# Kernel optimization log

Hardware: AMD Instinct MI355X
Metric: run time of the kernel (lower is better)

The kernel has to match this reference:

```python
import jax, jax.numpy as jnp
import numpy as np

B, H, S, DH = 2, 16, 2048, 64
MASK_FILL = -10000.0


def setup_inputs() -> dict:
    key = jax.random.key(0)
    kq, kk, kv = jax.random.split(key, 3)
    q = jax.random.normal(kq, (B, H, S, DH), dtype=jnp.float32)
    k = jax.random.normal(kk, (B, H, S, DH), dtype=jnp.float32)
    v = jax.random.normal(kv, (B, H, S, DH), dtype=jnp.float32)
    # causal mask: True where attention is disallowed (upper triangle)
    mask = jnp.triu(jnp.ones((S, S), dtype=jnp.bool_), k=1)
    return {"q": q, "k": k, "v": v, "mask": mask}


def reference(q, k, v, mask):
    scale = 1.0 / jnp.sqrt(jnp.asarray(k.shape[-1], dtype=q.dtype))
    # scores: [B, H, S_q, S_k]
    scores = jnp.einsum("bhqd,bhkd->bhqk", q, k) * scale
    # additive mask: masked_fill on a zeros [S_k, S_v] matrix -> -10000 where mask
    attn_bias = jnp.where(mask, jnp.asarray(MASK_FILL, dtype=k.dtype),
                          jnp.asarray(0.0, dtype=k.dtype))
    scores = scores + attn_bias  # broadcast over batch/heads
    attn = jax.nn.softmax(scores, axis=-1)
    # dropout_rate = 0.0 -> identity
    return jnp.einsum("bhqk,bhkd->bhqd", attn, v)
```

## Files before the change

### kernel.cpp

```cpp
#include <hip/hip_runtime.h>


#define S_LEN  2048
#define DHDIM  64
#define NHEADS 32
#define LDP    72
#define M2     23.083120654223414f
#define QSCALE 0.18033688011117658f
#define NSLOT  52

typedef __attribute__((ext_vector_type(8))) short bf16x8;
typedef __attribute__((ext_vector_type(4))) float f32x4;
typedef __attribute__((ext_vector_type(16))) float f32x16;

#define RT(qt,k0,k1,sl) ((unsigned)(qt)<<24 | (unsigned)(k0)<<16 | (unsigned)(k1)<<8 | (unsigned)(sl))
__device__ __constant__ unsigned RTAB[63] = {
    RT(31,0,11,49),  RT(31,11,22,50), RT(30,0,11,46),  RT(21,0,11,20),
    RT(21,11,22,21), RT(20,0,11,18),  RT(10,0,11,255),
    RT(31,22,32,51), RT(30,11,21,47), RT(30,21,31,48), RT(29,0,10,43),
    RT(29,10,20,44), RT(29,20,30,45), RT(28,0,10,40),  RT(28,10,20,41),
    RT(27,0,10,37),  RT(20,11,21,19), RT(19,0,10,16),  RT(19,10,20,17),
    RT(18,0,10,14),  RT(9,0,10,255),
    RT(28,20,29,42), RT(27,10,19,38), RT(27,19,28,39), RT(26,0,9,34),
    RT(26,9,18,35),  RT(26,18,27,36), RT(25,0,9,31),   RT(25,9,18,32),
    RT(24,0,9,28),   RT(18,10,19,15), RT(17,0,9,12),   RT(17,9,18,13),
    RT(16,0,9,10),   RT(8,0,9,255),
    RT(25,18,26,33), RT(24,9,17,29),  RT(24,17,25,30), RT(23,0,8,25),
    RT(23,8,16,26),  RT(23,16,24,27), RT(22,0,8,22),   RT(22,8,16,23),
    RT(16,9,17,11),  RT(15,0,8,8),    RT(15,8,16,9),   RT(14,0,8,6),
    RT(7,0,8,255),
    RT(22,16,23,24), RT(14,8,15,7),   RT(13,0,7,4),    RT(13,7,14,5),
    RT(12,0,7,2),    RT(6,0,7,255),
    RT(12,7,13,3),   RT(11,0,6,0),    RT(11,6,12,1),   RT(5,0,6,255),
    RT(4,0,5,255),   RT(3,0,4,255),   RT(2,0,3,255),   RT(1,0,2,255),
    RT(0,0,1,255)};

__device__ __forceinline__ float fast_exp2(float x) {
#if __has_builtin(__builtin_amdgcn_exp2f)
    return __builtin_amdgcn_exp2f(x);
#else
    return exp2f(x);
#endif
}
__device__ __forceinline__ unsigned short f2bf(float f) {
    unsigned u = __float_as_uint(f);
    return (unsigned short)((u + 0x7fffu + ((u >> 16) & 1u)) >> 16);
}
__device__ __forceinline__ void ld8(const float* p, float* f) {
    float4 a = *(const float4*)p, b = *(const float4*)(p + 4);
    f[0]=a.x; f[1]=a.y; f[2]=a.z; f[3]=a.w; f[4]=b.x; f[5]=b.y; f[6]=b.z; f[7]=b.w;
}
__device__ __forceinline__ uint4 pack8(const float* f, float scale) {
    union { uint4 v; unsigned short s[8]; } w;
    #pragma unroll
    for (int j = 0; j < 8; j++) w.s[j] = f2bf(f[j] * scale);
    return w.v;
}
__device__ __forceinline__ unsigned packhi(float a, float b) {
#if __has_builtin(__builtin_amdgcn_perm)
    return __builtin_amdgcn_perm(__float_as_uint(b), __float_as_uint(a), 0x07060302u);
#else
    return (__float_as_uint(a) >> 16) | (__float_as_uint(b) & 0xffff0000u);
#endif
}

__global__ __launch_bounds__(256) void prep(
    const float* __restrict__ Qf, const float* __restrict__ Kf,
    const float* __restrict__ Vf, unsigned short* __restrict__ qb,
    unsigned short* __restrict__ kb, unsigned short* __restrict__ vtb)
{
    const int st = blockIdx.x, bh = blockIdx.y;
    __shared__ unsigned lt32[64][LDP / 2];
    const float* vp = Vf + ((size_t)bh * S_LEN + st * 64) * DHDIM;
    {
        const int c = threadIdx.x;
        const int sp = c >> 3;
        const int d0 = (c & 7) * 8;
        float fa[8], fb[8];
        ld8(vp + (2 * sp) * DHDIM + d0, fa);
        ld8(vp + (2 * sp + 1) * DHDIM + d0, fb);
        #pragma unroll
        for (int j = 0; j < 8; j++) {
            int d = d0 + j;
            int colw = (sp & 3) | ((((sp >> 2) ^ (d >> 3)) & 7) << 2);
            lt32[d][colw] = (unsigned)f2bf(fa[j]) | ((unsigned)f2bf(fb[j]) << 16);
        }
    }
    size_t off = ((size_t)(bh * 32 + st) * 4096) + (size_t)threadIdx.x * 16;
    float f[8];
    ld8(Qf + off, f);     *(uint4*)(qb + off)     = pack8(f, QSCALE);
    ld8(Qf + off + 8, f); *(uint4*)(qb + off + 8) = pack8(f, QSCALE);
    ld8(Kf + off, f);     *(uint4*)(kb + off)     = pack8(f, 1.0f);
    ld8(Kf + off + 8, f); *(uint4*)(kb + off + 8) = pack8(f, 1.0f);
    __syncthreads();
    unsigned short* op = vtb + (size_t)bh * DHDIM * S_LEN + st * 64;
    for (int c = threadIdx.x; c < 512; c += 256) {
        int d = c >> 3, q = c & 7;
        int colw = ((q ^ (d >> 3)) & 7) << 2;
        *(uint4*)(op + (size_t)d * S_LEN + q * 8) = *(const uint4*)&lt32[d][colw];
    }
}

__global__ __launch_bounds__(256, 3) void fattn_splitk(
    const unsigned short* __restrict__ Qp, const unsigned short* __restrict__ Kp,
    const unsigned short* __restrict__ Vp,
    float* __restrict__ pO, float* __restrict__ pL, float* __restrict__ O)
{
    __shared__ unsigned short smem[320 * LDP];
    unsigned short (*ks)[LDP]   = (unsigned short(*)[LDP])smem;
    unsigned short (*vtsA)[LDP] = (unsigned short(*)[LDP])(smem + 64 * LDP);
    unsigned short (*vtsB)[LDP] = (unsigned short(*)[LDP])(smem + 128 * LDP);
    unsigned short (*pstA)[LDP] = (unsigned short(*)[LDP])(smem + 192 * LDP);
    unsigned short (*pstB)[LDP] = (unsigned short(*)[LDP])(smem + 256 * LDP);

    const int bh   = blockIdx.x;
    const unsigned e = RTAB[blockIdx.y];
    const int qt   = e >> 24;
    const int k0   = (e >> 16) & 255;
    const int k1   = (e >> 8) & 255;
    const int sl   = e & 255;
    const bool whole = (sl == 255);

    const int tid  = threadIdx.x;
    const int wave = tid >> 6, lane = tid & 63;
    const int q31  = lane & 31, hi = lane >> 5;
    const int qh   = wave & 1, kh = wave >> 1;
    const int qrow = qh * 32 + q31;

    const unsigned short* qsrc = Qp + ((size_t)bh * S_LEN + qt * 64 + qrow) * DHDIM;
    const bf16x8 bq0 = *(const bf16x8*)(qsrc + hi * 8);
    const bf16x8 bq1 = *(const bf16x8*)(qsrc + 16 + hi * 8);
    const bf16x8 bq2 = *(const bf16x8*)(qsrc + 32 + hi * 8);
    const bf16x8 bq3 = *(const bf16x8*)(qsrc + 48 + hi * 8);

    bf16x8 ones;
    #pragma unroll
    for (int j = 0; j < 8; j++) ones[j] = (short)0x3F80;

    f32x16 of, ofl;
    #pragma unroll
    for (int i = 0; i < 16; i++) { of[i] = 0.f; ofl[i] = 0.f; }
    unsigned pdw[8];

    const unsigned short* Kbh = Kp + (size_t)bh * S_LEN * DHDIM;
    const unsigned short* Vbh = Vp + (size_t)bh * DHDIM * S_LEN;
    const int sr = tid >> 3, sc = (tid & 7) * 8;
    uint4 kr0, kr1, vr0, vr1;
    {
        const unsigned short* ksrc = Kbh + (size_t)k0 * 64 * DHDIM;
        const unsigned short* vsrc = Vbh + k0 * 64;
        kr0 = *(const uint4*)(ksrc + sr * DHDIM + sc);
        kr1 = *(const uint4*)(ksrc + (sr + 32) * DHDIM + sc);
        vr0 = *(const uint4*)(vsrc + (size_t)sr * S_LEN + sc);
        vr1 = *(const uint4*)(vsrc + (size_t)(sr + 32) * S_LEN + sc);
    }

    for (int kt = k0; kt < k1; kt++) {
        __syncthreads();

        *(uint4*)&ks[sr][sc]      = kr0;
        *(uint4*)&ks[sr + 32][sc] = kr1;
        {
            unsigned short (*vts)[LDP] = (kt & 1) ? vtsB : vtsA;
            *(uint4*)&vts[sr][sc]      = vr0;
            *(uint4*)&vts[sr + 32][sc] = vr1;
        }
        if (kt > k0) {
            unsigned short (*pst)[LDP] = ((kt - 1) & 1) ? pstB : pstA;
            const int cb = kh * 32 + 4 * hi;
            *(uint2*)&pst[qrow][cb +  0] = *(uint2*)&pdw[0];
            *(uint2*)&pst[qrow][cb +  8] = *(uint2*)&pdw[2];
            *(uint2*)&pst[qrow][cb + 16] = *(uint2*)&pdw[4];
            *(uint2*)&pst[qrow][cb + 24] = *(uint2*)&pdw[6];
        }
        if (kt + 1 < k1) {
            const unsigned short* ksrc = Kbh + (size_t)(kt + 1) * 64 * DHDIM;
            const unsigned short* vsrc = Vbh + (kt + 1) * 64;
            kr0 = *(const uint4*)(ksrc + sr * DHDIM + sc);
            kr1 = *(const uint4*)(ksrc + (sr + 32) * DHDIM + sc);
            vr0 = *(const uint4*)(vsrc + (size_t)sr * S_LEN + sc);
            vr1 = *(const uint4*)(vsrc + (size_t)(sr + 32) * S_LEN + sc);
        }
        __syncthreads();

        if (kt > k0) {
            const unsigned short (*pst)[LDP] = ((kt - 1) & 1) ? pstB : pstA;
            const unsigned short (*vts)[LDP] = ((kt - 1) & 1) ? vtsB : vtsA;
            __builtin_amdgcn_s_setprio(1);
            #pragma unroll
            for (int s = 0; s < 4; s++) {
                bf16x8 av = *(const bf16x8*)&vts[kh * 32 + q31][s * 16 + hi * 8];
                bf16x8 bp = *(const bf16x8*)&pst[qrow][s * 16 + hi * 8];
                of  = __builtin_amdgcn_mfma_f32_32x32x16_bf16(av, bp, of, 0, 0, 0);
                ofl = __builtin_amdgcn_mfma_f32_32x32x16_bf16(ones, bp, ofl, 0, 0, 0);
            }
            __builtin_amdgcn_s_setprio(0);
        }

        f32x16 sf;
        #pragma unroll
        for (int i = 0; i < 16; i++) sf[i] = -M2;
        __builtin_amdgcn_s_setprio(1);
        {
            bf16x8 ak = *(const bf16x8*)&ks[kh * 32 + q31][hi * 8];
            sf = __builtin_amdgcn_mfma_f32_32x32x16_bf16(ak, bq0, sf, 0, 0, 0);
            ak = *(const bf16x8*)&ks[kh * 32 + q31][16 + hi * 8];
            sf = __builtin_amdgcn_mfma_f32_32x32x16_bf16(ak, bq1, sf, 0, 0, 0);
            ak = *(const bf16x8*)&ks[kh * 32 + q31][32 + hi * 8];
            sf = __builtin_amdgcn_mfma_f32_32x32x16_bf16(ak, bq2, sf, 0, 0, 0);
            ak = *(const bf16x8*)&ks[kh * 32 + q31][48 + hi * 8];
            sf = __builtin_amdgcn_mfma_f32_32x32x16_bf16(ak, bq3, sf, 0, 0, 0);
        }
        __builtin_amdgcn_s_setprio(0);

        const bool diag = (kt == qt);
        #pragma unroll
        for (int g = 0; g < 4; g++) {
            float p[4];
            #pragma unroll
            for (int r2 = 0; r2 < 4; r2++) {
                float pv = fast_exp2(sf[g * 4 + r2]);
                if (diag) {
                    const int kl = kh * 32 + 8 * g + 4 * hi + r2;
                    if (kl > qrow) pv = 0.f;
                }
                p[r2] = pv;
            }
            pdw[g * 2]     = packhi(p[0], p[1]);
            pdw[g * 2 + 1] = packhi(p[2], p[3]);
        }
    }

    {
        unsigned short (*pst)[LDP] = ((k1 - 1) & 1) ? pstB : pstA;
        const int cb = kh * 32 + 4 * hi;
        *(uint2*)&pst[qrow][cb +  0] = *(uint2*)&pdw[0];
        *(uint2*)&pst[qrow][cb +  8] = *(uint2*)&pdw[2];
        *(uint2*)&pst[qrow][cb + 16] = *(uint2*)&pdw[4];
        *(uint2*)&pst[qrow][cb + 24] = *(uint2*)&pdw[6];
        __syncthreads();
        const unsigned short (*pstc)[LDP] = ((k1 - 1) & 1) ? pstB : pstA;
        const unsigned short (*vts)[LDP]  = ((k1 - 1) & 1) ? vtsB : vtsA;
        __builtin_amdgcn_s_setprio(1);
        #pragma unroll
        for (int s = 0; s < 4; s++) {
            bf16x8 av = *(const bf16x8*)&vts[kh * 32 + q31][s * 16 + hi * 8];
            bf16x8 bp = *(const bf16x8*)&pstc[qrow][s * 16 + hi * 8];
            of  = __builtin_amdgcn_mfma_f32_32x32x16_bf16(av, bp, of, 0, 0, 0);
            ofl = __builtin_amdgcn_mfma_f32_32x32x16_bf16(ones, bp, ofl, 0, 0, 0);
        }
        __builtin_amdgcn_s_setprio(0);
    }

    const float l = ofl[0];
    if (whole) {
        const float inv = 1.f / l;
        float* op = O + ((size_t)bh * S_LEN + qt * 64 + qrow) * DHDIM
                  + kh * 32 + 4 * hi;
        #pragma unroll
        for (int g = 0; g < 4; g++)
            *(float4*)(op + 8 * g) = make_float4(
                of[4 * g] * inv, of[4 * g + 1] * inv,
                of[4 * g + 2] * inv, of[4 * g + 3] * inv);
    } else {
        const int slot = bh * NSLOT + sl;
        if (kh == 0 && hi == 0) pL[slot * 64 + qrow] = l;
        float* op = pO + (size_t)slot * 4096 + qrow * 64 + kh * 32 + 4 * hi;
        #pragma unroll
        for (int g = 0; g < 4; g++)
            *(float4*)(op + 8 * g) = make_float4(
                of[4 * g], of[4 * g + 1], of[4 * g + 2], of[4 * g + 3]);
    }
}

__global__ __launch_bounds__(256) void combine(
    const float* __restrict__ pO, const float* __restrict__ pL,
    float* __restrict__ O)
{
    const int qt = 11 + blockIdx.x, bh = blockIdx.y;
    int base, cnt;
    if (qt < 22) { base = (qt - 11) * 2;      cnt = 2; }
    else         { base = 22 + 3 * (qt - 22); cnt = 3; }
    const int sb = bh * NSLOT + base;
    const float* A = pO + (size_t)sb * 4096;
    float* out = O + ((size_t)bh * S_LEN + qt * 64) * DHDIM;
    #pragma unroll
    for (int k = 0; k < 4; k++) {
        int c = threadIdx.x + k * 256;
        int row = c >> 4;
        float l = pL[sb * 64 + row] + pL[(sb + 1) * 64 + row];
        float4 a = *(const float4*)(A + c * 4);
        float4 b = *(const float4*)(A + 4096 + c * 4);
        float4 s = make_float4(a.x + b.x, a.y + b.y, a.z + b.z, a.w + b.w);
        if (cnt == 3) {
            l += pL[(sb + 2) * 64 + row];
            float4 d = *(const float4*)(A + 8192 + c * 4);
            s = make_float4(s.x + d.x, s.y + d.y, s.z + d.z, s.w + d.w);
        }
        float inv = 1.f / l;
        *(float4*)(out + c * 4) = make_float4(
            s.x * inv, s.y * inv, s.z * inv, s.w * inv);
    }
}

template <bool PRE>
__global__ __launch_bounds__(256) void fattn_kernel(
    const void* __restrict__ Qp, const void* __restrict__ Kp,
    const void* __restrict__ Vp, float* __restrict__ O)
{
    __shared__ unsigned short smem[192 * LDP];
    unsigned short (*ks)[LDP]  = (unsigned short(*)[LDP])smem;
    unsigned short (*vts)[LDP] = (unsigned short(*)[LDP])(smem + 64 * LDP);
    unsigned short (*qs)[LDP]  = (unsigned short(*)[LDP])(smem + 128 * LDP);
    unsigned short (*pst)[LDP] = qs;

    const int id = blockIdx.y * 32 + blockIdx.x;
    const int g  = id >> 8;
    const int r8 = id & 255;
    const int bh = r8 >> 3;
    const int s8 = r8 & 7;
    const int qt = (g == 0) ? 31 - 2 * s8 : (g == 1) ? 2 * s8
                 : (g == 2) ? 30 - 2 * s8 : 2 * s8 + 1;

    const int tid = threadIdx.x;
    const int wave = tid >> 6, lane = tid & 63;
    const int quad = lane >> 4, l16 = lane & 15;

    if constexpr (PRE) {
        const unsigned short* src = (const unsigned short*)Qp
            + ((size_t)bh * S_LEN + qt * 64) * DHDIM;
        for (int c = tid; c < 512; c += 256) {
            int row = c >> 3, c8 = (c & 7) * 8;
            *(uint4*)&qs[row][c8] = *(const uint4*)(src + row * DHDIM + c8);
        }
    } else {
        const float* src = (const float*)Qp + ((size_t)bh * S_LEN + qt * 64) * DHDIM;
        for (int c = tid; c < 512; c += 256) {
            int row = c >> 3, c8 = (c & 7) * 8;
            float f[8]; ld8(src + row * DHDIM + c8, f);
            *(uint4*)&qs[row][c8] = pack8(f, QSCALE);
        }
    }
    __syncthreads();

    const int prow = wave * 16 + l16;
    const bf16x8 bq0 = *(const bf16x8*)&qs[prow][quad * 8];
    const bf16x8 bq1 = *(const bf16x8*)&qs[prow][32 + quad * 8];

    float l_p = 0.f;
    f32x4 of[4];
    #pragma unroll
    for (int n = 0; n < 4; n++) of[n] = (f32x4){0.f, 0.f, 0.f, 0.f};

    for (int kt = 0; kt <= qt; kt++) {
        __syncthreads();
        if constexpr (PRE) {
            const unsigned short* ksrc = (const unsigned short*)Kp
                + ((size_t)bh * S_LEN + kt * 64) * DHDIM;
            const unsigned short* vsrc = (const unsigned short*)Vp
                + (size_t)bh * DHDIM * S_LEN + kt * 64;
            for (int c = tid; c < 512; c += 256) {
                int row = c >> 3, c8 = (c & 7) * 8;
                *(uint4*)&ks[row][c8]  = *(const uint4*)(ksrc + row * DHDIM + c8);
                *(uint4*)&vts[row][c8] = *(const uint4*)(vsrc + (size_t)row * S_LEN + c8);
            }
        } else {
            const float* ksrc = (const float*)Kp + ((size_t)bh * S_LEN + kt * 64) * DHDIM;
            const float* vsrc = (const float*)Vp + ((size_t)bh * S_LEN + kt * 64) * DHDIM;
            for (int c = tid; c < 512; c += 256) {
                int row = c >> 3, c8 = (c & 7) * 8;
                float f[8];
                ld8(ksrc + row * DHDIM + c8, f);
                *(uint4*)&ks[row][c8] = pack8(f, 1.0f);
                ld8(vsrc + row * DHDIM + c8, f);
                #pragma unroll
                for (int j = 0; j < 8; j++) vts[c8 + j][row] = f2bf(f[j]);
            }
        }
        __syncthreads();

        f32x4 sf[4];
        #pragma unroll
        for (int n = 0; n < 4; n++) {
            bf16x8 ak0 = *(const bf16x8*)&ks[n * 16 + l16][quad * 8];
            bf16x8 ak1 = *(const bf16x8*)&ks[n * 16 + l16][32 + quad * 8];
            sf[n] = (f32x4){-M2, -M2, -M2, -M2};
            sf[n] = __builtin_amdgcn_mfma_f32_16x16x32_bf16(ak0, bq0, sf[n], 0, 0, 0);
            sf[n] = __builtin_amdgcn_mfma_f32_16x16x32_bf16(ak1, bq1, sf[n], 0, 0, 0);
        }

        const bool diag = (kt == qt);
        #pragma unroll
        for (int n = 0; n < 4; n++) {
            float p[4];
            #pragma unroll
            for (int r = 0; r < 4; r++) {
                p[r] = fast_exp2(sf[n][r]);
                if (diag && (n * 16 + quad * 4 + r > prow)) p[r] = 0.f;
                l_p += p[r];
            }
            uint2 dw;
            dw.x = packhi(p[0], p[1]);
            dw.y = packhi(p[2], p[3]);
            *(uint2*)&pst[prow][n * 16 + quad * 4] = dw;
        }
        asm volatile("s_waitcnt lgkmcnt(0)" ::: "memory");

        bf16x8 bp0 = *(const bf16x8*)&pst[prow][quad * 8];
        bf16x8 bp1 = *(const bf16x8*)&pst[prow][32 + quad * 8];
        #pragma unroll
        for (int n = 0; n < 4; n++) {
            bf16x8 av0 = *(const bf16x8*)&vts[n * 16 + l16][quad * 8];
            bf16x8 av1 = *(const bf16x8*)&vts[n * 16 + l16][32 + quad * 8];
            of[n] = __builtin_amdgcn_mfma_f32_16x16x32_bf16(av0, bp0, of[n], 0, 0, 0);
            of[n] = __builtin_amdgcn_mfma_f32_16x16x32_bf16(av1, bp1, of[n], 0, 0, 0);
        }
    }

    l_p += __shfl_xor(l_p, 16);
    l_p += __shfl_xor(l_p, 32);
    const float inv = 1.f / l_p;
    float* op = O + ((size_t)bh * S_LEN + qt * 64 + prow) * DHDIM;
    #pragma unroll
    for (int n = 0; n < 4; n++)
        *(float4*)(op + n * 16 + quad * 4) = make_float4(
            of[n][0] * inv, of[n][1] * inv, of[n][2] * inv, of[n][3] * inv);
}

extern "C" void kernel_launch(void* const* d_in, const int* in_sizes, int n_in,
                              void* d_out, int out_size, void* d_ws, size_t ws_size,
                              hipStream_t stream) {
    const float* Q = (const float*)d_in[0];
    const float* K = (const float*)d_in[1];
    const float* V = (const float*)d_in[2];
    float* O = (float*)d_out;
    const size_t N = (size_t)NHEADS * S_LEN * DHDIM;
    const size_t prepB  = 3 * N * sizeof(unsigned short);
    const size_t partB  = (size_t)NSLOT * 32 * (4096 + 64) * sizeof(float);

    if (d_ws && ws_size >= prepB + partB) {
        unsigned short* qb  = (unsigned short*)d_ws;
        unsigned short* kb  = qb + N;
        unsigned short* vtb = kb + N;
        float* pO = (float*)((char*)d_ws + prepB);
        float* pL = pO + (size_t)NSLOT * 32 * 4096;
        prep<<<dim3(S_LEN / 64, NHEADS), 256, 0, stream>>>(Q, K, V, qb, kb, vtb);
        fattn_splitk<<<dim3(32, 63), 256, 0, stream>>>(qb, kb, vtb, pO, pL, O);
        combine<<<dim3(21, 32), 256, 0, stream>>>(pO, pL, O);
    } else if (d_ws && ws_size >= prepB) {
        unsigned short* qb  = (unsigned short*)d_ws;
        unsigned short* kb  = qb + N;
        unsigned short* vtb = kb + N;
        prep<<<dim3(S_LEN / 64, NHEADS), 256, 0, stream>>>(Q, K, V, qb, kb, vtb);
        fattn_kernel<true><<<dim3(32, 32), 256, 0, stream>>>(qb, kb, vtb, O);
    } else {
        fattn_kernel<false><<<dim3(32, 32), 256, 0, stream>>>(Q, K, V, O);
    }
}
```

Before: 141.7 us.

## Keep P in registers via lane shuffles and double-buffer K/V tiles

```diff
diff --git a/kernel.cpp b/kernel.cpp
--- a/kernel.cpp
+++ b/kernel.cpp
@@ -63,6 +63,12 @@
     return (__float_as_uint(a) >> 16) | (__float_as_uint(b) & 0xffff0000u);
 #endif
 }
+__device__ __forceinline__ bf16x8 mk_bf16x8(unsigned d0, unsigned d1,
+                                            unsigned d2, unsigned d3) {
+    union { unsigned u[4]; bf16x8 v; } w;
+    w.u[0] = d0; w.u[1] = d1; w.u[2] = d2; w.u[3] = d3;
+    return w.v;
+}
 
 __global__ __launch_bounds__(256) void prep(
     const float* __restrict__ Qf, const float* __restrict__ Kf,
@@ -101,17 +107,16 @@
     }
 }
 
-__global__ __launch_bounds__(256, 3) void fattn_splitk(
+__global__ __launch_bounds__(256) void fattn_splitk(
     const unsigned short* __restrict__ Qp, const unsigned short* __restrict__ Kp,
     const unsigned short* __restrict__ Vp,
     float* __restrict__ pO, float* __restrict__ pL, float* __restrict__ O)
 {
-    __shared__ unsigned short smem[320 * LDP];
-    unsigned short (*ks)[LDP]   = (unsigned short(*)[LDP])smem;
-    unsigned short (*vtsA)[LDP] = (unsigned short(*)[LDP])(smem + 64 * LDP);
-    unsigned short (*vtsB)[LDP] = (unsigned short(*)[LDP])(smem + 128 * LDP);
-    unsigned short (*pstA)[LDP] = (unsigned short(*)[LDP])(smem + 192 * LDP);
-    unsigned short (*pstB)[LDP] = (unsigned short(*)[LDP])(smem + 256 * LDP);
+    __shared__ unsigned short smem[256 * LDP];
+    unsigned short (*ksA)[LDP]  = (unsigned short(*)[LDP])smem;
+    unsigned short (*ksB)[LDP]  = (unsigned short(*)[LDP])(smem + 64 * LDP);
+    unsigned short (*vtsA)[LDP] = (unsigned short(*)[LDP])(smem + 128 * LDP);
+    unsigned short (*vtsB)[LDP] = (unsigned short(*)[LDP])(smem + 192 * LDP);
 
     const int bh   = blockIdx.x;
     const unsigned e = RTAB[blockIdx.y];
@@ -133,14 +138,10 @@
     const bf16x8 bq2 = *(const bf16x8*)(qsrc + 32 + hi * 8);
     const bf16x8 bq3 = *(const bf16x8*)(qsrc + 48 + hi * 8);
 
-    bf16x8 ones;
+    f32x16 of2[2];
     #pragma unroll
-    for (int j = 0; j < 8; j++) ones[j] = (short)0x3F80;
-
-    f32x16 of, ofl;
-    #pragma unroll
-    for (int i = 0; i < 16; i++) { of[i] = 0.f; ofl[i] = 0.f; }
-    unsigned pdw[8];
+    for (int i = 0; i < 16; i++) { of2[0][i] = 0.f; of2[1][i] = 0.f; }
+    float l_p = 0.f;
 
     const unsigned short* Kbh = Kp + (size_t)bh * S_LEN * DHDIM;
     const unsigned short* Vbh = Vp + (size_t)bh * DHDIM * S_LEN;
@@ -154,66 +155,64 @@
         vr0 = *(const uint4*)(vsrc + (size_t)sr * S_LEN + sc);
         vr1 = *(const uint4*)(vsrc + (size_t)(sr + 32) * S_LEN + sc);
     }
+    {
+        unsigned short (*ks)[LDP]  = (k0 & 1) ? ksB : ksA;
+        unsigned short (*vts)[LDP] = (k0 & 1) ? vtsB : vtsA;
+        *(uint4*)&ks[sr][sc]       = kr0;
+        *(uint4*)&ks[sr + 32][sc]  = kr1;
+        *(uint4*)&vts[sr][sc]      = vr0;
+        *(uint4*)&vts[sr + 32][sc] = vr1;
+    }
+    if (k0 + 1 < k1) {
+        const unsigned short* ksrc = Kbh + (size_t)(k0 + 1) * 64 * DHDIM;
+        const unsigned short* vsrc = Vbh + (k0 + 1) * 64;
+        kr0 = *(const uint4*)(ksrc + sr * DHDIM + sc);
+        kr1 = *(const uint4*)(ksrc + (sr + 32) * DHDIM + sc);
+        vr0 = *(const uint4*)(vsrc + (size_t)sr * S_LEN + sc);
+        vr1 = *(const uint4*)(vsrc + (size_t)(sr + 32) * S_LEN + sc);
+    }
 
     for (int kt = k0; kt < k1; kt++) {
         __syncthreads();
 
-        *(uint4*)&ks[sr][sc]      = kr0;
-        *(uint4*)&ks[sr + 32][sc] = kr1;
-        {
-            unsigned short (*vts)[LDP] = (kt & 1) ? vtsB : vtsA;
+        if (kt + 1 < k1) {
+            unsigned short (*ks)[LDP]  = ((kt + 1) & 1) ? ksB : ksA;
+            unsigned short (*vts)[LDP] = ((kt + 1) & 1) ? vtsB : vtsA;
+            *(uint4*)&ks[sr][sc]       = kr0;
+            *(uint4*)&ks[sr + 32][sc]  = kr1;
             *(uint4*)&vts[sr][sc]      = vr0;
             *(uint4*)&vts[sr + 32][sc] = vr1;
-        }
-        if (kt > k0) {
-            unsigned short (*pst)[LDP] = ((kt - 1) & 1) ? pstB : pstA;
-            const int cb = kh * 32 + 4 * hi;
-            *(uint2*)&pst[qrow][cb +  0] = *(uint2*)&pdw[0];
-            *(uint2*)&pst[qrow][cb +  8] = *(uint2*)&pdw[2];
-            *(uint2*)&pst[qrow][cb + 16] = *(uint2*)&pdw[4];
-            *(uint2*)&pst[qrow][cb + 24] = *(uint2*)&pdw[6];
-        }
-        if (kt + 1 < k1) {
-            const unsigned short* ksrc = Kbh + (size_t)(kt + 1) * 64 * DHDIM;
-            const unsigned short* vsrc = Vbh + (kt + 1) * 64;
-            kr0 = *(const uint4*)(ksrc + sr * DHDIM + sc);
-            kr1 = *(const uint4*)(ksrc + (sr + 32) * DHDIM + sc);
-            vr0 = *(const uint4*)(vsrc + (size_t)sr * S_LEN + sc);
-            vr1 = *(const uint4*)(vsrc + (size_t)(sr + 32) * S_LEN + sc);
-        }
-        __syncthreads();
-
-        if (kt > k0) {
-            const unsigned short (*pst)[LDP] = ((kt - 1) & 1) ? pstB : pstA;
-            const unsigned short (*vts)[LDP] = ((kt - 1) & 1) ? vtsB : vtsA;
-            __builtin_amdgcn_s_setprio(1);
-            #pragma unroll
-            for (int s = 0; s < 4; s++) {
-                bf16x8 av = *(const bf16x8*)&vts[kh * 32 + q31][s * 16 + hi * 8];
-                bf16x8 bp = *(const bf16x8*)&pst[qrow][s * 16 + hi * 8];
-                of  = __builtin_amdgcn_mfma_f32_32x32x16_bf16(av, bp, of, 0, 0, 0);
-                ofl = __builtin_amdgcn_mfma_f32_32x32x16_bf16(ones, bp, ofl, 0, 0, 0);
-            }
-            __builtin_amdgcn_s_setprio(0);
-        }
+            if (kt + 2 < k1) {
+                const unsigned short* ksrc = Kbh + (size_t)(kt + 2) * 64 * DHDIM;
+                const unsigned short* vsrc = Vbh + (kt + 2) * 64;
+                kr0 = *(const uint4*)(ksrc + sr * DHDIM + sc);
+                kr1 = *(const uint4*)(ksrc + (sr + 32) * DHDIM + sc);
+                vr0 = *(const uint4*)(vsrc + (size_t)sr * S_LEN + sc);
+                vr1 = *(const uint4*)(vsrc + (size_t)(sr + 32) * S_LEN + sc);
+            }
+        }
+
+        const unsigned short (*ksc)[LDP] = (kt & 1) ? ksB : ksA;
+        const unsigned short (*vtc)[LDP] = (kt & 1) ? vtsB : vtsA;
 
         f32x16 sf;
         #pragma unroll
         for (int i = 0; i < 16; i++) sf[i] = -M2;
         __builtin_amdgcn_s_setprio(1);
         {
-            bf16x8 ak = *(const bf16x8*)&ks[kh * 32 + q31][hi * 8];
+            bf16x8 ak = *(const bf16x8*)&ksc[kh * 32 + q31][hi * 8];
             sf = __builtin_amdgcn_mfma_f32_32x32x16_bf16(ak, bq0, sf, 0, 0, 0);
-            ak = *(const bf16x8*)&ks[kh * 32 + q31][16 + hi * 8];
+            ak = *(const bf16x8*)&ksc[kh * 32 + q31][16 + hi * 8];
             sf = __builtin_amdgcn_mfma_f32_32x32x16_bf16(ak, bq1, sf, 0, 0, 0);
-            ak = *(const bf16x8*)&ks[kh * 32 + q31][32 + hi * 8];
+            ak = *(const bf16x8*)&ksc[kh * 32 + q31][32 + hi * 8];
             sf = __builtin_amdgcn_mfma_f32_32x32x16_bf16(ak, bq2, sf, 0, 0, 0);
-            ak = *(const bf16x8*)&ks[kh * 32 + q31][48 + hi * 8];
+            ak = *(const bf16x8*)&ksc[kh * 32 + q31][48 + hi * 8];
             sf = __builtin_amdgcn_mfma_f32_32x32x16_bf16(ak, bq3, sf, 0, 0, 0);
         }
         __builtin_amdgcn_s_setprio(0);
 
         const bool diag = (kt == qt);
+        unsigned pdw[8];
         #pragma unroll
         for (int g = 0; g < 4; g++) {
             float p[4];
@@ -225,51 +224,80 @@
                     if (kl > qrow) pv = 0.f;
                 }
                 p[r2] = pv;
+                l_p += pv;
             }
             pdw[g * 2]     = packhi(p[0], p[1]);
             pdw[g * 2 + 1] = packhi(p[2], p[3]);
         }
-    }
-
-    {
-        unsigned short (*pst)[LDP] = ((k1 - 1) & 1) ? pstB : pstA;
-        const int cb = kh * 32 + 4 * hi;
-        *(uint2*)&pst[qrow][cb +  0] = *(uint2*)&pdw[0];
-        *(uint2*)&pst[qrow][cb +  8] = *(uint2*)&pdw[2];
-        *(uint2*)&pst[qrow][cb + 16] = *(uint2*)&pdw[4];
-        *(uint2*)&pst[qrow][cb + 24] = *(uint2*)&pdw[6];
-        __syncthreads();
-        const unsigned short (*pstc)[LDP] = ((k1 - 1) & 1) ? pstB : pstA;
-        const unsigned short (*vts)[LDP]  = ((k1 - 1) & 1) ? vtsB : vtsA;
+
         __builtin_amdgcn_s_setprio(1);
         #pragma unroll
-        for (int s = 0; s < 4; s++) {
-            bf16x8 av = *(const bf16x8*)&vts[kh * 32 + q31][s * 16 + hi * 8];
-            bf16x8 bp = *(const bf16x8*)&pstc[qrow][s * 16 + hi * 8];
-            of  = __builtin_amdgcn_mfma_f32_32x32x16_bf16(av, bp, of, 0, 0, 0);
-            ofl = __builtin_amdgcn_mfma_f32_32x32x16_bf16(ones, bp, ofl, 0, 0, 0);
+        for (int js = 0; js < 2; js++) {
+            const unsigned a0 = pdw[4 * js],     a1 = pdw[4 * js + 1];
+            const unsigned b0 = pdw[4 * js + 2], b1 = pdw[4 * js + 3];
+            const unsigned pa0 = __shfl_xor(a0, 32), pa1 = __shfl_xor(a1, 32);
+            const unsigned pb0 = __shfl_xor(b0, 32), pb1 = __shfl_xor(b1, 32);
+            const bf16x8 bp = mk_bf16x8(hi ? pb0 : a0, hi ? pb1 : a1,
+                                        hi ? b0 : pa0, hi ? b1 : pa1);
+            const int scol = (2 * kh + js) * 16 + hi * 8;
+            bf16x8 av = *(const bf16x8*)&vtc[q31][scol];
+            of2[0] = __builtin_amdgcn_mfma_f32_32x32x16_bf16(av, bp, of2[0], 0, 0, 0);
+            av = *(const bf16x8*)&vtc[32 + q31][scol];
+            of2[1] = __builtin_amdgcn_mfma_f32_32x32x16_bf16(av, bp, of2[1], 0, 0, 0);
         }
         __builtin_amdgcn_s_setprio(0);
     }
 
-    const float l = ofl[0];
-    if (whole) {
-        const float inv = 1.f / l;
-        float* op = O + ((size_t)bh * S_LEN + qt * 64 + qrow) * DHDIM
-                  + kh * 32 + 4 * hi;
-        #pragma unroll
-        for (int g = 0; g < 4; g++)
-            *(float4*)(op + 8 * g) = make_float4(
-                of[4 * g] * inv, of[4 * g + 1] * inv,
-                of[4 * g + 2] * inv, of[4 * g + 3] * inv);
-    } else {
-        const int slot = bh * NSLOT + sl;
-        if (kh == 0 && hi == 0) pL[slot * 64 + qrow] = l;
-        float* op = pO + (size_t)slot * 4096 + qrow * 64 + kh * 32 + 4 * hi;
-        #pragma unroll
-        for (int g = 0; g < 4; g++)
-            *(float4*)(op + 8 * g) = make_float4(
-                of[4 * g], of[4 * g + 1], of[4 * g + 2], of[4 * g + 3]);
+    float l2 = l_p + __shfl_xor(l_p, 32);
+    __syncthreads();
+    float* fs = (float*)smem;
+    const int base = (qh * 64 + lane) * 36;
+    if (kh == 1) {
+        #pragma unroll
+        for (int dh = 0; dh < 2; dh++)
+            #pragma unroll
+            for (int g = 0; g < 4; g++)
+                *(float4*)&fs[base + dh * 16 + g * 4] = make_float4(
+                    of2[dh][4 * g], of2[dh][4 * g + 1],
+                    of2[dh][4 * g + 2], of2[dh][4 * g + 3]);
+        fs[base + 32] = l2;
+    }
+    __syncthreads();
+    if (kh == 0) {
+        #pragma unroll
+        for (int dh = 0; dh < 2; dh++)
+            #pragma unroll
+            for (int g = 0; g < 4; g++) {
+                float4 a = *(const float4*)&fs[base + dh * 16 + g * 4];
+                of2[dh][4 * g]     += a.x;
+                of2[dh][4 * g + 1] += a.y;
+                of2[dh][4 * g + 2] += a.z;
+                of2[dh][4 * g + 3] += a.w;
+            }
+        l2 += fs[base + 32];
+
+        if (whole) {
+            const float inv = 1.f / l2;
+            float* op = O + ((size_t)bh * S_LEN + qt * 64 + qrow) * DHDIM;
+            #pragma unroll
+            for (int dh = 0; dh < 2; dh++)
+                #pragma unroll
+                for (int g = 0; g < 4; g++)
+                    *(float4*)(op + dh * 32 + 8 * g + 4 * hi) = make_float4(
+                        of2[dh][4 * g] * inv, of2[dh][4 * g + 1] * inv,
+                        of2[dh][4 * g + 2] * inv, of2[dh][4 * g + 3] * inv);
+        } else {
+            const int slot = bh * NSLOT + sl;
+            if (hi == 0) pL[slot * 64 + qrow] = l2;
+            float* op = pO + (size_t)slot * 4096 + qrow * 64;
+            #pragma unroll
+            for (int dh = 0; dh < 2; dh++)
+                #pragma unroll
+                for (int g = 0; g < 4; g++)
+                    *(float4*)(op + dh * 32 + 8 * g + 4 * hi) = make_float4(
+                        of2[dh][4 * g], of2[dh][4 * g + 1],
+                        of2[dh][4 * g + 2], of2[dh][4 * g + 3]);
+        }
     }
 }
 
```

After: 139.7 us. Within noise of the previous version (-1.4%).
